# Optimization experiments

Measured on AMD Instinct MI355X. Metric: run time of the kernel, lower is better.

Reference implementation:

```python
import jax, jax.numpy as jnp
import numpy as np

N_NODES = 100000
N_EDGES = 1600000
F_IN = 128
F_OUT = 32


def setup_inputs() -> dict:
    key = jax.random.key(0)
    k1, k2, k3 = jax.random.split(key, 3)
    x = jax.random.normal(k1, (N_NODES, F_IN), dtype=jnp.float32)
    edge_index = jax.random.randint(k2, (2, N_EDGES), 0, N_NODES, dtype=jnp.int64)
    # Glorot-style init for the GCNConv linear weight [F_IN, F_OUT]
    W = jax.random.normal(k3, (F_IN, F_OUT), dtype=jnp.float32) * (1.0 / np.sqrt(F_IN))
    b = jnp.zeros((F_OUT,), dtype=jnp.float32)
    return {"x": x, "edge_index": edge_index, "W": W, "b": b}


def reference(x, edge_index, W, b):
    N = x.shape[0]
    # --- add self loops (PyG GCNConv default) ---
    loops = jnp.arange(N, dtype=edge_index.dtype)
    src = jnp.concatenate([edge_index[0], loops])  # message sources j
    dst = jnp.concatenate([edge_index[1], loops])  # aggregation targets i
    # --- symmetric normalization: deg^-1/2[src] * deg^-1/2[dst] ---
    ones = jnp.ones(src.shape[0], dtype=x.dtype)
    deg = jax.ops.segment_sum(ones, dst, num_segments=N)  # in-degree incl. self loop
    dinv = jnp.where(deg > 0, jax.lax.rsqrt(deg), jnp.zeros_like(deg))
    norm = dinv[src] * dinv[dst]  # [E+N]
    # --- linear transform then gather-scale-scatter aggregate ---
    h = x @ W  # [N, F_OUT]
    msgs = h[src] * norm[:, None]  # [E+N, F_OUT]
    out = jax.ops.segment_sum(msgs, dst, num_segments=N)  # [N, F_OUT]
    return out + b
```

## Files before the change

kernel.cpp:

```cpp
#include <hip/hip_runtime.h>
#include <hip/hip_fp16.h>

#define N_NODES 100000
#define N_EDGES 1600000
#define F_IN    128
#define F_OUT   32

#define BKT_SHIFT  7
#define BKT_SIZE   128
#define NBKT       782
#define BKT_STRIDE 2560

#define BIN_THREADS 512
#define BIN_TILE    8192
#define EPT         (BIN_TILE / BIN_THREADS)
#define NTILES      ((N_EDGES + BIN_TILE - 1) / BIN_TILE)

typedef _Float16 f16x8 __attribute__((ext_vector_type(8)));
typedef float    f32x4 __attribute__((ext_vector_type(4)));

__global__ __launch_bounds__(BIN_THREADS) void bin_kernel(const int* __restrict__ ei,
                                                          int* __restrict__ gcur,
                                                          unsigned int* __restrict__ binned) {
    __shared__ int cnt[NBKT], gbase[NBKT];
    int t = threadIdx.x;
    for (int b = t; b < NBKT; b += BIN_THREADS) cnt[b] = 0;
    __syncthreads();
    int ebase = blockIdx.x * BIN_TILE;
    unsigned int pk[EPT];
    int rk[EPT];
    short bkt[EPT];
#pragma unroll
    for (int k = 0; k < EPT; ++k) {
        int e = ebase + k * BIN_THREADS + t;
        if (e < N_EDGES) {
            int s = ei[e];
            int d = ei[N_EDGES + e];
            bkt[k] = (short)(d >> BKT_SHIFT);
            pk[k]  = (unsigned)s | ((unsigned)(d & (BKT_SIZE - 1)) << 25);
            rk[k]  = atomicAdd(&cnt[bkt[k]], 1);
        } else {
            bkt[k] = -1;
        }
    }
    __syncthreads();
    for (int b = t; b < NBKT; b += BIN_THREADS)
        if (cnt[b] > 0) gbase[b] = atomicAdd(&gcur[b], cnt[b]);
    __syncthreads();
#pragma unroll
    for (int k = 0; k < EPT; ++k) {
        if (bkt[k] >= 0) {
            int p = gbase[bkt[k]] + rk[k];
            if (p < BKT_STRIDE)
                binned[(size_t)bkt[k] * BKT_STRIDE + p] = pk[k];
        }
    }
}

#define WH_STRIDE 136
__global__ __launch_bounds__(512) void matmul_kernel(const float4* __restrict__ x4,
                                                     const float* __restrict__ W,
                                                     const unsigned int* __restrict__ binned,
                                                     const int* __restrict__ gcur,
                                                     __half* __restrict__ hs) {
    __shared__ _Float16 Wh[F_OUT * WH_STRIDE];
    __shared__ int cnt128[BKT_SIZE];
    __shared__ float dinvL[BKT_SIZE];
    int t = threadIdx.x;
    int b = blockIdx.x;

    if (t < BKT_SIZE) cnt128[t] = 0;
    {
        int col = t & 31, kb = (t >> 5) * 8;
        for (int u = 0; u < 8; ++u)
            Wh[col * WH_STRIDE + kb + u] = (_Float16)W[(kb + u) * F_OUT + col];
    }
    __syncthreads();

    int ne = gcur[b];
    if (ne > BKT_STRIDE) ne = BKT_STRIDE;
    const unsigned int* eb = binned + (size_t)b * BKT_STRIDE;
    for (int i = t; i < ne; i += 512)
        atomicAdd(&cnt128[eb[i] >> 25], 1);
    __syncthreads();
    if (t < BKT_SIZE) dinvL[t] = rsqrtf((float)(cnt128[t] + 1));
    __syncthreads();

    int w = t >> 6, l = t & 63;
    int lr = l & 15, kg = l >> 4;
    int row = b * 128 + w * 16 + lr;
    const float4* xr = x4 + (size_t)row * 32;
    bool rok = row < N_NODES;

    f16x8 a[4];
#pragma unroll
    for (int ks = 0; ks < 4; ++ks) {
        float4 v0, v1;
        if (rok) {
            v0 = xr[ks * 8 + kg * 2];
            v1 = xr[ks * 8 + kg * 2 + 1];
        } else {
            v0 = make_float4(0, 0, 0, 0);
            v1 = v0;
        }
        f16x8 av;
        av[0] = (_Float16)v0.x; av[1] = (_Float16)v0.y;
        av[2] = (_Float16)v0.z; av[3] = (_Float16)v0.w;
        av[4] = (_Float16)v1.x; av[5] = (_Float16)v1.y;
        av[6] = (_Float16)v1.z; av[7] = (_Float16)v1.w;
        a[ks] = av;
    }

    f32x4 c0 = {0.f, 0.f, 0.f, 0.f}, c1 = {0.f, 0.f, 0.f, 0.f};
#pragma unroll
    for (int ks = 0; ks < 4; ++ks) {
        f16x8 b0 = *(const f16x8*)&Wh[lr * WH_STRIDE + ks * 32 + kg * 8];
        f16x8 b1 = *(const f16x8*)&Wh[(16 + lr) * WH_STRIDE + ks * 32 + kg * 8];
        c0 = __builtin_amdgcn_mfma_f32_16x16x32_f16(a[ks], b0, c0, 0, 0, 0);
        c1 = __builtin_amdgcn_mfma_f32_16x16x32_f16(a[ks], b1, c1, 0, 0, 0);
    }

    int lrow0 = w * 16 + kg * 4;
#pragma unroll
    for (int i = 0; i < 4; ++i) {
        int orow = b * 128 + lrow0 + i;
        if (orow < N_NODES) {
            float dv = dinvL[lrow0 + i];
            hs[(size_t)orow * F_OUT + lr]      = (__half)(c0[i] * dv);
            hs[(size_t)orow * F_OUT + 16 + lr] = (__half)(c1[i] * dv);
        }
    }
}

__device__ inline void acc8(uint4 u, float* a) {
    float2 f0 = __half22float2(*(__half2*)&u.x);
    float2 f1 = __half22float2(*(__half2*)&u.y);
    float2 f2 = __half22float2(*(__half2*)&u.z);
    float2 f3 = __half22float2(*(__half2*)&u.w);
    a[0] += f0.x; a[1] += f0.y; a[2] += f1.x; a[3] += f1.y;
    a[4] += f2.x; a[5] += f2.y; a[6] += f3.x; a[7] += f3.y;
}

#define AEPT 5
__global__ __launch_bounds__(512) void aggregate_kernel(const unsigned int* __restrict__ binned,
                                                        const int* __restrict__ gcur,
                                                        const uint4* __restrict__ hs8,
                                                        const float* __restrict__ bias,
                                                        float* __restrict__ out) {
    __shared__ int cnt[BKT_SIZE];
    __shared__ int sc[BKT_SIZE];
    __shared__ int rp[BKT_SIZE + 1];
    __shared__ int se[BKT_STRIDE];
    int t = threadIdx.x;
    int b = blockIdx.x;
    int ne = gcur[b];
    if (ne > BKT_STRIDE) ne = BKT_STRIDE;
    const unsigned int* eb = binned + (size_t)b * BKT_STRIDE;

    if (t < BKT_SIZE) cnt[t] = 0;
    __syncthreads();

    unsigned pk[AEPT];
    int rk[AEPT];
#pragma unroll
    for (int k = 0; k < AEPT; ++k) {
        int i = t + k * 512;
        pk[k] = (i < ne) ? eb[i] : 0xFFFFFFFFu;
    }
#pragma unroll
    for (int k = 0; k < AEPT; ++k) {
        rk[k] = -1;
        if (pk[k] != 0xFFFFFFFFu)
            rk[k] = atomicAdd(&cnt[pk[k] >> 25], 1);
    }
    __syncthreads();
    int v = (t < BKT_SIZE) ? cnt[t] : 0;
    if (t < BKT_SIZE) sc[t] = v;
    __syncthreads();
    for (int off = 1; off < BKT_SIZE; off <<= 1) {
        int add = (t < BKT_SIZE && t >= off) ? sc[t - off] : 0;
        __syncthreads();
        if (t < BKT_SIZE) sc[t] += add;
        __syncthreads();
    }
    if (t < BKT_SIZE) rp[t] = sc[t] - v;
    if (t == 0) rp[BKT_SIZE] = ne;
    __syncthreads();
#pragma unroll
    for (int k = 0; k < AEPT; ++k) {
        if (rk[k] >= 0) {
            int pos = rp[pk[k] >> 25] + rk[k];
            se[pos] = (int)(pk[k] & 0x1FFFFFF);
        }
    }
    __syncthreads();

    int n = t >> 2, q = t & 3;
    int gnode = b * BKT_SIZE + n;
    if (gnode >= N_NODES) return;
    int beg = rp[n], end = rp[n + 1];
    int deg = end - beg;
    float acc[8] = {0.f, 0.f, 0.f, 0.f, 0.f, 0.f, 0.f, 0.f};
    int p = beg;
    for (; p + 7 < end; p += 8) {
        uint4 u0 = hs8[(size_t)se[p]     * 4 + q];
        uint4 u1 = hs8[(size_t)se[p + 1] * 4 + q];
        uint4 u2 = hs8[(size_t)se[p + 2] * 4 + q];
        uint4 u3 = hs8[(size_t)se[p + 3] * 4 + q];
        uint4 u4 = hs8[(size_t)se[p + 4] * 4 + q];
        uint4 u5 = hs8[(size_t)se[p + 5] * 4 + q];
        uint4 u6 = hs8[(size_t)se[p + 6] * 4 + q];
        uint4 u7 = hs8[(size_t)se[p + 7] * 4 + q];
        acc8(u0, acc); acc8(u1, acc); acc8(u2, acc); acc8(u3, acc);
        acc8(u4, acc); acc8(u5, acc); acc8(u6, acc); acc8(u7, acc);
    }
    for (; p + 3 < end; p += 4) {
        uint4 u0 = hs8[(size_t)se[p]     * 4 + q];
        uint4 u1 = hs8[(size_t)se[p + 1] * 4 + q];
        uint4 u2 = hs8[(size_t)se[p + 2] * 4 + q];
        uint4 u3 = hs8[(size_t)se[p + 3] * 4 + q];
        acc8(u0, acc); acc8(u1, acc); acc8(u2, acc); acc8(u3, acc);
    }
    for (; p < end; ++p)
        acc8(hs8[(size_t)se[p] * 4 + q], acc);

    float dv = rsqrtf((float)(deg + 1));
    uint4 us = hs8[(size_t)gnode * 4 + q];
    float selfv[8];
    {
        float2 f0 = __half22float2(*(__half2*)&us.x);
        float2 f1 = __half22float2(*(__half2*)&us.y);
        float2 f2 = __half22float2(*(__half2*)&us.z);
        float2 f3 = __half22float2(*(__half2*)&us.w);
        selfv[0] = f0.x; selfv[1] = f0.y; selfv[2] = f1.x; selfv[3] = f1.y;
        selfv[4] = f2.x; selfv[5] = f2.y; selfv[6] = f3.x; selfv[7] = f3.y;
    }
    float4 bv0 = *(const float4*)&bias[q * 8];
    float4 bv1 = *(const float4*)&bias[q * 8 + 4];
    float4 o0, o1;
    o0.x = bv0.x + dv * (acc[0] + selfv[0]);
    o0.y = bv0.y + dv * (acc[1] + selfv[1]);
    o0.z = bv0.z + dv * (acc[2] + selfv[2]);
    o0.w = bv0.w + dv * (acc[3] + selfv[3]);
    o1.x = bv1.x + dv * (acc[4] + selfv[4]);
    o1.y = bv1.y + dv * (acc[5] + selfv[5]);
    o1.z = bv1.z + dv * (acc[6] + selfv[6]);
    o1.w = bv1.w + dv * (acc[7] + selfv[7]);
    *(float4*)&out[(size_t)gnode * F_OUT + q * 8]     = o0;
    *(float4*)&out[(size_t)gnode * F_OUT + q * 8 + 4] = o1;
}

extern "C" void kernel_launch(void* const* d_in, const int* in_sizes, int n_in,
                              void* d_out, int out_size, void* d_ws, size_t ws_size,
                              hipStream_t stream) {
    const float* x  = (const float*)d_in[0];
    const int*   ei = (const int*)d_in[1];
    const float* W  = (const float*)d_in[2];
    const float* b  = (const float*)d_in[3];
    float* out = (float*)d_out;

    int*          gcur   = (int*)d_ws;
    unsigned int* binned = (unsigned int*)(gcur + 1024);
    __half*       hs     = (__half*)(binned + (size_t)NBKT * BKT_STRIDE);

    hipMemsetAsync(gcur, 0, NBKT * sizeof(int), stream);

    bin_kernel<<<NTILES, BIN_THREADS, 0, stream>>>(ei, gcur, binned);

    matmul_kernel<<<NBKT, 512, 0, stream>>>((const float4*)x, W, binned, gcur, hs);

    aggregate_kernel<<<NBKT, 512, 0, stream>>>(binned, gcur, (const uint4*)hs, b, out);
}
```

Measured before the change: 70.82 us.

## Co-schedule binning with matmul, split sort into own kernel, apply dinv per edge

```diff
diff --git a/kernel.cpp b/kernel.cpp
--- a/kernel.cpp
+++ b/kernel.cpp
@@ -10,147 +10,125 @@
 #define BKT_SIZE   128
 #define NBKT       782
 #define BKT_STRIDE 2560
+#define RP_STRIDE  132
 
 #define BIN_THREADS 512
 #define BIN_TILE    8192
-#define EPT         (BIN_TILE / BIN_THREADS)
+#define EPT         16
 #define NTILES      ((N_EDGES + BIN_TILE - 1) / BIN_TILE)
 
 typedef _Float16 f16x8 __attribute__((ext_vector_type(8)));
 typedef float    f32x4 __attribute__((ext_vector_type(4)));
 
-__global__ __launch_bounds__(BIN_THREADS) void bin_kernel(const int* __restrict__ ei,
-                                                          int* __restrict__ gcur,
-                                                          unsigned int* __restrict__ binned) {
-    __shared__ int cnt[NBKT], gbase[NBKT];
+#define WH_STRIDE 136
+
+__global__ __launch_bounds__(512) void fused_bin_matmul_kernel(const int* __restrict__ ei,
+                                                               int* __restrict__ gcur,
+                                                               unsigned int* __restrict__ binned,
+                                                               const float4* __restrict__ x4,
+                                                               const float* __restrict__ W,
+                                                               __half* __restrict__ hs) {
+    __shared__ char pool[9216];
     int t = threadIdx.x;
-    for (int b = t; b < NBKT; b += BIN_THREADS) cnt[b] = 0;
-    __syncthreads();
-    int ebase = blockIdx.x * BIN_TILE;
-    unsigned int pk[EPT];
-    int rk[EPT];
-    short bkt[EPT];
-#pragma unroll
-    for (int k = 0; k < EPT; ++k) {
-        int e = ebase + k * BIN_THREADS + t;
-        if (e < N_EDGES) {
-            int s = ei[e];
-            int d = ei[N_EDGES + e];
-            bkt[k] = (short)(d >> BKT_SHIFT);
-            pk[k]  = (unsigned)s | ((unsigned)(d & (BKT_SIZE - 1)) << 25);
-            rk[k]  = atomicAdd(&cnt[bkt[k]], 1);
-        } else {
-            bkt[k] = -1;
-        }
-    }
-    __syncthreads();
-    for (int b = t; b < NBKT; b += BIN_THREADS)
-        if (cnt[b] > 0) gbase[b] = atomicAdd(&gcur[b], cnt[b]);
-    __syncthreads();
-#pragma unroll
-    for (int k = 0; k < EPT; ++k) {
-        if (bkt[k] >= 0) {
-            int p = gbase[bkt[k]] + rk[k];
-            if (p < BKT_STRIDE)
-                binned[(size_t)bkt[k] * BKT_STRIDE + p] = pk[k];
-        }
-    }
-}
-
-#define WH_STRIDE 136
-__global__ __launch_bounds__(512) void matmul_kernel(const float4* __restrict__ x4,
-                                                     const float* __restrict__ W,
-                                                     const unsigned int* __restrict__ binned,
-                                                     const int* __restrict__ gcur,
-                                                     __half* __restrict__ hs) {
-    __shared__ _Float16 Wh[F_OUT * WH_STRIDE];
-    __shared__ int cnt128[BKT_SIZE];
-    __shared__ float dinvL[BKT_SIZE];
-    int t = threadIdx.x;
-    int b = blockIdx.x;
-
-    if (t < BKT_SIZE) cnt128[t] = 0;
-    {
-        int col = t & 31, kb = (t >> 5) * 8;
-        for (int u = 0; u < 8; ++u)
-            Wh[col * WH_STRIDE + kb + u] = (_Float16)W[(kb + u) * F_OUT + col];
-    }
-    __syncthreads();
-
-    int ne = gcur[b];
-    if (ne > BKT_STRIDE) ne = BKT_STRIDE;
-    const unsigned int* eb = binned + (size_t)b * BKT_STRIDE;
-    for (int i = t; i < ne; i += 512)
-        atomicAdd(&cnt128[eb[i] >> 25], 1);
-    __syncthreads();
-    if (t < BKT_SIZE) dinvL[t] = rsqrtf((float)(cnt128[t] + 1));
-    __syncthreads();
-
-    int w = t >> 6, l = t & 63;
-    int lr = l & 15, kg = l >> 4;
-    int row = b * 128 + w * 16 + lr;
-    const float4* xr = x4 + (size_t)row * 32;
-    bool rok = row < N_NODES;
-
-    f16x8 a[4];
-#pragma unroll
-    for (int ks = 0; ks < 4; ++ks) {
-        float4 v0, v1;
-        if (rok) {
-            v0 = xr[ks * 8 + kg * 2];
-            v1 = xr[ks * 8 + kg * 2 + 1];
-        } else {
-            v0 = make_float4(0, 0, 0, 0);
-            v1 = v0;
-        }
-        f16x8 av;
-        av[0] = (_Float16)v0.x; av[1] = (_Float16)v0.y;
-        av[2] = (_Float16)v0.z; av[3] = (_Float16)v0.w;
-        av[4] = (_Float16)v1.x; av[5] = (_Float16)v1.y;
-        av[6] = (_Float16)v1.z; av[7] = (_Float16)v1.w;
-        a[ks] = av;
-    }
-
-    f32x4 c0 = {0.f, 0.f, 0.f, 0.f}, c1 = {0.f, 0.f, 0.f, 0.f};
-#pragma unroll
-    for (int ks = 0; ks < 4; ++ks) {
-        f16x8 b0 = *(const f16x8*)&Wh[lr * WH_STRIDE + ks * 32 + kg * 8];
-        f16x8 b1 = *(const f16x8*)&Wh[(16 + lr) * WH_STRIDE + ks * 32 + kg * 8];
-        c0 = __builtin_amdgcn_mfma_f32_16x16x32_f16(a[ks], b0, c0, 0, 0, 0);
-        c1 = __builtin_amdgcn_mfma_f32_16x16x32_f16(a[ks], b1, c1, 0, 0, 0);
-    }
-
-    int lrow0 = w * 16 + kg * 4;
-#pragma unroll
-    for (int i = 0; i < 4; ++i) {
-        int orow = b * 128 + lrow0 + i;
-        if (orow < N_NODES) {
-            float dv = dinvL[lrow0 + i];
-            hs[(size_t)orow * F_OUT + lr]      = (__half)(c0[i] * dv);
-            hs[(size_t)orow * F_OUT + 16 + lr] = (__half)(c1[i] * dv);
-        }
-    }
-}
-
-__device__ inline void acc8(uint4 u, float* a) {
-    float2 f0 = __half22float2(*(__half2*)&u.x);
-    float2 f1 = __half22float2(*(__half2*)&u.y);
-    float2 f2 = __half22float2(*(__half2*)&u.z);
-    float2 f3 = __half22float2(*(__half2*)&u.w);
-    a[0] += f0.x; a[1] += f0.y; a[2] += f1.x; a[3] += f1.y;
-    a[4] += f2.x; a[5] += f2.y; a[6] += f3.x; a[7] += f3.y;
-}
-
-#define AEPT 5
-__global__ __launch_bounds__(512) void aggregate_kernel(const unsigned int* __restrict__ binned,
-                                                        const int* __restrict__ gcur,
-                                                        const uint4* __restrict__ hs8,
-                                                        const float* __restrict__ bias,
-                                                        float* __restrict__ out) {
+
+    if (blockIdx.x < NTILES) {
+        int* cnt   = (int*)pool;
+        int* gbase = cnt + NBKT;
+        for (int b = t; b < NBKT; b += BIN_THREADS) cnt[b] = 0;
+        __syncthreads();
+        int ebase = blockIdx.x * BIN_TILE;
+        unsigned int pk[EPT];
+        int rk[EPT];
+        short bkt[EPT];
+#pragma unroll
+        for (int k = 0; k < EPT; ++k) {
+            int e = ebase + k * BIN_THREADS + t;
+            if (e < N_EDGES) {
+                int s = ei[e];
+                int d = ei[N_EDGES + e];
+                bkt[k] = (short)(d >> BKT_SHIFT);
+                pk[k]  = (unsigned)s | ((unsigned)(d & (BKT_SIZE - 1)) << 25);
+                rk[k]  = atomicAdd(&cnt[bkt[k]], 1);
+            } else {
+                bkt[k] = -1;
+            }
+        }
+        __syncthreads();
+        for (int b = t; b < NBKT; b += BIN_THREADS)
+            if (cnt[b] > 0) gbase[b] = atomicAdd(&gcur[b], cnt[b]);
+        __syncthreads();
+#pragma unroll
+        for (int k = 0; k < EPT; ++k) {
+            if (bkt[k] >= 0) {
+                int p = gbase[bkt[k]] + rk[k];
+                if (p < BKT_STRIDE)
+                    binned[(size_t)bkt[k] * BKT_STRIDE + p] = pk[k];
+            }
+        }
+    } else {
+        _Float16* Wh = (_Float16*)pool;
+        int b = blockIdx.x - NTILES;
+        {
+            int col = t & 31, kb = (t >> 5) * 8;
+            for (int u = 0; u < 8; ++u)
+                Wh[col * WH_STRIDE + kb + u] = (_Float16)W[(kb + u) * F_OUT + col];
+        }
+        __syncthreads();
+
+        int w = t >> 6, l = t & 63;
+        int lr = l & 15, kg = l >> 4;
+        int row = b * 128 + w * 16 + lr;
+        const float4* xr = x4 + (size_t)row * 32;
+        bool rok = row < N_NODES;
+
+        f16x8 a[4];
+#pragma unroll
+        for (int ks = 0; ks < 4; ++ks) {
+            float4 v0, v1;
+            if (rok) {
+                v0 = xr[ks * 8 + kg * 2];
+                v1 = xr[ks * 8 + kg * 2 + 1];
+            } else {
+                v0 = make_float4(0, 0, 0, 0);
+                v1 = v0;
+            }
+            f16x8 av;
+            av[0] = (_Float16)v0.x; av[1] = (_Float16)v0.y;
+            av[2] = (_Float16)v0.z; av[3] = (_Float16)v0.w;
+            av[4] = (_Float16)v1.x; av[5] = (_Float16)v1.y;
+            av[6] = (_Float16)v1.z; av[7] = (_Float16)v1.w;
+            a[ks] = av;
+        }
+
+        f32x4 c0 = {0.f, 0.f, 0.f, 0.f}, c1 = {0.f, 0.f, 0.f, 0.f};
+#pragma unroll
+        for (int ks = 0; ks < 4; ++ks) {
+            f16x8 b0 = *(const f16x8*)&Wh[lr * WH_STRIDE + ks * 32 + kg * 8];
+            f16x8 b1 = *(const f16x8*)&Wh[(16 + lr) * WH_STRIDE + ks * 32 + kg * 8];
+            c0 = __builtin_amdgcn_mfma_f32_16x16x32_f16(a[ks], b0, c0, 0, 0, 0);
+            c1 = __builtin_amdgcn_mfma_f32_16x16x32_f16(a[ks], b1, c1, 0, 0, 0);
+        }
+
+        int lrow0 = w * 16 + kg * 4;
+#pragma unroll
+        for (int i = 0; i < 4; ++i) {
+            int orow = b * 128 + lrow0 + i;
+            if (orow < N_NODES) {
+                hs[(size_t)orow * F_OUT + lr]      = (__half)c0[i];
+                hs[(size_t)orow * F_OUT + 16 + lr] = (__half)c1[i];
+            }
+        }
+    }
+}
+
+__global__ __launch_bounds__(256) void sort_kernel(const unsigned int* __restrict__ binned,
+                                                   const int* __restrict__ gcur,
+                                                   int* __restrict__ se_g,
+                                                   int* __restrict__ rowptr,
+                                                   float* __restrict__ dinv) {
     __shared__ int cnt[BKT_SIZE];
     __shared__ int sc[BKT_SIZE];
     __shared__ int rp[BKT_SIZE + 1];
-    __shared__ int se[BKT_STRIDE];
     int t = threadIdx.x;
     int b = blockIdx.x;
     int ne = gcur[b];
@@ -160,15 +138,15 @@
     if (t < BKT_SIZE) cnt[t] = 0;
     __syncthreads();
 
-    unsigned pk[AEPT];
-    int rk[AEPT];
-#pragma unroll
-    for (int k = 0; k < AEPT; ++k) {
-        int i = t + k * 512;
+    unsigned pk[10];
+    int rk[10];
+#pragma unroll
+    for (int k = 0; k < 10; ++k) {
+        int i = t + k * 256;
         pk[k] = (i < ne) ? eb[i] : 0xFFFFFFFFu;
     }
 #pragma unroll
-    for (int k = 0; k < AEPT; ++k) {
+    for (int k = 0; k < 10; ++k) {
         rk[k] = -1;
         if (pk[k] != 0xFFFFFFFFu)
             rk[k] = atomicAdd(&cnt[pk[k] >> 25], 1);
@@ -186,68 +164,86 @@
     if (t < BKT_SIZE) rp[t] = sc[t] - v;
     if (t == 0) rp[BKT_SIZE] = ne;
     __syncthreads();
-#pragma unroll
-    for (int k = 0; k < AEPT; ++k) {
+
+    int gnode = b * BKT_SIZE + t;
+    if (t < BKT_SIZE && gnode < N_NODES)
+        dinv[gnode] = rsqrtf((float)(cnt[t] + 1));
+    if (t <= BKT_SIZE)
+        rowptr[b * RP_STRIDE + t] = rp[t];
+
+    int* se = se_g + (size_t)b * BKT_STRIDE;
+#pragma unroll
+    for (int k = 0; k < 10; ++k) {
         if (rk[k] >= 0) {
             int pos = rp[pk[k] >> 25] + rk[k];
             se[pos] = (int)(pk[k] & 0x1FFFFFF);
         }
     }
-    __syncthreads();
-
-    int n = t >> 2, q = t & 3;
+}
+
+__global__ __launch_bounds__(256) void aggregate_kernel(const int* __restrict__ se_g,
+                                                        const int* __restrict__ rowptr,
+                                                        const float* __restrict__ dinv,
+                                                        const uint2* __restrict__ hs4,
+                                                        const float* __restrict__ bias,
+                                                        float* __restrict__ out) {
+    int t = threadIdx.x;
+    int b   = blockIdx.x >> 2;
+    int sub = blockIdx.x & 3;
+    int n = sub * 32 + (t >> 3);
+    int j4 = t & 7;
     int gnode = b * BKT_SIZE + n;
     if (gnode >= N_NODES) return;
-    int beg = rp[n], end = rp[n + 1];
+    int beg = rowptr[b * RP_STRIDE + n];
+    int end = rowptr[b * RP_STRIDE + n + 1];
     int deg = end - beg;
-    float acc[8] = {0.f, 0.f, 0.f, 0.f, 0.f, 0.f, 0.f, 0.f};
+    const int* se = se_g + (size_t)b * BKT_STRIDE;
+
+    float a0 = 0.f, a1 = 0.f, a2 = 0.f, a3 = 0.f;
     int p = beg;
     for (; p + 7 < end; p += 8) {
-        uint4 u0 = hs8[(size_t)se[p]     * 4 + q];
-        uint4 u1 = hs8[(size_t)se[p + 1] * 4 + q];
-        uint4 u2 = hs8[(size_t)se[p + 2] * 4 + q];
-        uint4 u3 = hs8[(size_t)se[p + 3] * 4 + q];
-        uint4 u4 = hs8[(size_t)se[p + 4] * 4 + q];
-        uint4 u5 = hs8[(size_t)se[p + 5] * 4 + q];
-        uint4 u6 = hs8[(size_t)se[p + 6] * 4 + q];
-        uint4 u7 = hs8[(size_t)se[p + 7] * 4 + q];
-        acc8(u0, acc); acc8(u1, acc); acc8(u2, acc); acc8(u3, acc);
-        acc8(u4, acc); acc8(u5, acc); acc8(u6, acc); acc8(u7, acc);
-    }
-    for (; p + 3 < end; p += 4) {
-        uint4 u0 = hs8[(size_t)se[p]     * 4 + q];
-        uint4 u1 = hs8[(size_t)se[p + 1] * 4 + q];
-        uint4 u2 = hs8[(size_t)se[p + 2] * 4 + q];
-        uint4 u3 = hs8[(size_t)se[p + 3] * 4 + q];
-        acc8(u0, acc); acc8(u1, acc); acc8(u2, acc); acc8(u3, acc);
-    }
-    for (; p < end; ++p)
-        acc8(hs8[(size_t)se[p] * 4 + q], acc);
+        int s0 = se[p],     s1 = se[p + 1], s2 = se[p + 2], s3 = se[p + 3];
+        int s4 = se[p + 4], s5 = se[p + 5], s6 = se[p + 6], s7 = se[p + 7];
+        uint2 u0 = hs4[(size_t)s0 * 8 + j4]; float w0 = dinv[s0];
+        uint2 u1 = hs4[(size_t)s1 * 8 + j4]; float w1 = dinv[s1];
+        uint2 u2 = hs4[(size_t)s2 * 8 + j4]; float w2 = dinv[s2];
+        uint2 u3 = hs4[(size_t)s3 * 8 + j4]; float w3 = dinv[s3];
+        uint2 u4 = hs4[(size_t)s4 * 8 + j4]; float w4 = dinv[s4];
+        uint2 u5 = hs4[(size_t)s5 * 8 + j4]; float w5 = dinv[s5];
+        uint2 u6 = hs4[(size_t)s6 * 8 + j4]; float w6 = dinv[s6];
+        uint2 u7 = hs4[(size_t)s7 * 8 + j4]; float w7 = dinv[s7];
+#define FMA4(u, w) { \
+        float2 f0 = __half22float2(*(__half2*)&(u).x); \
+        float2 f1 = __half22float2(*(__half2*)&(u).y); \
+        a0 = fmaf(f0.x, (w), a0); a1 = fmaf(f0.y, (w), a1); \
+        a2 = fmaf(f1.x, (w), a2); a3 = fmaf(f1.y, (w), a3); }
+        FMA4(u0, w0) FMA4(u1, w1) FMA4(u2, w2) FMA4(u3, w3)
+        FMA4(u4, w4) FMA4(u5, w5) FMA4(u6, w6) FMA4(u7, w7)
+    }
+    for (; p + 1 < end; p += 2) {
+        int s0 = se[p], s1 = se[p + 1];
+        uint2 u0 = hs4[(size_t)s0 * 8 + j4]; float w0 = dinv[s0];
+        uint2 u1 = hs4[(size_t)s1 * 8 + j4]; float w1 = dinv[s1];
+        FMA4(u0, w0) FMA4(u1, w1)
+    }
+    if (p < end) {
+        int s0 = se[p];
+        uint2 u0 = hs4[(size_t)s0 * 8 + j4]; float w0 = dinv[s0];
+        FMA4(u0, w0)
+    }
+#undef FMA4
 
     float dv = rsqrtf((float)(deg + 1));
-    uint4 us = hs8[(size_t)gnode * 4 + q];
-    float selfv[8];
-    {
-        float2 f0 = __half22float2(*(__half2*)&us.x);
-        float2 f1 = __half22float2(*(__half2*)&us.y);
-        float2 f2 = __half22float2(*(__half2*)&us.z);
-        float2 f3 = __half22float2(*(__half2*)&us.w);
-        selfv[0] = f0.x; selfv[1] = f0.y; selfv[2] = f1.x; selfv[3] = f1.y;
-        selfv[4] = f2.x; selfv[5] = f2.y; selfv[6] = f3.x; selfv[7] = f3.y;
-    }
-    float4 bv0 = *(const float4*)&bias[q * 8];
-    float4 bv1 = *(const float4*)&bias[q * 8 + 4];
-    float4 o0, o1;
-    o0.x = bv0.x + dv * (acc[0] + selfv[0]);
-    o0.y = bv0.y + dv * (acc[1] + selfv[1]);
-    o0.z = bv0.z + dv * (acc[2] + selfv[2]);
-    o0.w = bv0.w + dv * (acc[3] + selfv[3]);
-    o1.x = bv1.x + dv * (acc[4] + selfv[4]);
-    o1.y = bv1.y + dv * (acc[5] + selfv[5]);
-    o1.z = bv1.z + dv * (acc[6] + selfv[6]);
-    o1.w = bv1.w + dv * (acc[7] + selfv[7]);
-    *(float4*)&out[(size_t)gnode * F_OUT + q * 8]     = o0;
-    *(float4*)&out[(size_t)gnode * F_OUT + q * 8 + 4] = o1;
+    uint2 us = hs4[(size_t)gnode * 8 + j4];
+    float2 s0 = __half22float2(*(__half2*)&us.x);
+    float2 s1 = __half22float2(*(__half2*)&us.y);
+    float4 bv = *(const float4*)&bias[j4 * 4];
+    float4 o;
+    o.x = bv.x + dv * (a0 + dv * s0.x);
+    o.y = bv.y + dv * (a1 + dv * s0.y);
+    o.z = bv.z + dv * (a2 + dv * s1.x);
+    o.w = bv.w + dv * (a3 + dv * s1.y);
+    *(float4*)&out[(size_t)gnode * F_OUT + j4 * 4] = o;
 }
 
 extern "C" void kernel_launch(void* const* d_in, const int* in_sizes, int n_in,
@@ -261,13 +257,17 @@
 
     int*          gcur   = (int*)d_ws;
     unsigned int* binned = (unsigned int*)(gcur + 1024);
-    __half*       hs     = (__half*)(binned + (size_t)NBKT * BKT_STRIDE);
+    int*          se_g   = (int*)(binned + (size_t)NBKT * BKT_STRIDE);
+    int*          rowptr = se_g + (size_t)NBKT * BKT_STRIDE;
+    float*        dinv   = (float*)(rowptr + NBKT * RP_STRIDE);
+    __half*       hs     = (__half*)(dinv + ((N_NODES + 3) & ~3));
 
     hipMemsetAsync(gcur, 0, NBKT * sizeof(int), stream);
 
-    bin_kernel<<<NTILES, BIN_THREADS, 0, stream>>>(ei, gcur, binned);
-
-    matmul_kernel<<<NBKT, 512, 0, stream>>>((const float4*)x, W, binned, gcur, hs);
-
-    aggregate_kernel<<<NBKT, 512, 0, stream>>>(binned, gcur, (const uint4*)hs, b, out);
-}
+    fused_bin_matmul_kernel<<<NTILES + NBKT, 512, 0, stream>>>(ei, gcur, binned,
+                                                               (const float4*)x, W, hs);
+
+    sort_kernel<<<NBKT, 256, 0, stream>>>(binned, gcur, se_g, rowptr, dinv);
+
+    aggregate_kernel<<<NBKT * 4, 256, 0, stream>>>(se_g, rowptr, dinv, (const uint2*)hs, b, out);
+}
```

New measurement: 80.31 us. 13.4% more time.

## Split aggregation of each bucket across two 256-thread blocks

Applied to the files above, without the earlier changes.

```diff
diff --git a/kernel.cpp b/kernel.cpp
--- a/kernel.cpp
+++ b/kernel.cpp
@@ -15,6 +15,10 @@
 #define BIN_TILE    8192
 #define EPT         (BIN_TILE / BIN_THREADS)
 #define NTILES      ((N_EDGES + BIN_TILE - 1) / BIN_TILE)
+
+#define AGG_SPLIT  2
+#define SUB        64
+#define SUB_STRIDE 1408
 
 typedef _Float16 f16x8 __attribute__((ext_vector_type(8)));
 typedef float    f32x4 __attribute__((ext_vector_type(4)));
@@ -141,65 +145,76 @@
     a[4] += f2.x; a[5] += f2.y; a[6] += f3.x; a[7] += f3.y;
 }
 
-#define AEPT 5
-__global__ __launch_bounds__(512) void aggregate_kernel(const unsigned int* __restrict__ binned,
+__global__ __launch_bounds__(256) void aggregate_kernel(const unsigned int* __restrict__ binned,
                                                         const int* __restrict__ gcur,
                                                         const uint4* __restrict__ hs8,
                                                         const float* __restrict__ bias,
                                                         float* __restrict__ out) {
-    __shared__ int cnt[BKT_SIZE];
-    __shared__ int sc[BKT_SIZE];
-    __shared__ int rp[BKT_SIZE + 1];
-    __shared__ int se[BKT_STRIDE];
+    __shared__ int cnt[SUB];
+    __shared__ int sc[SUB];
+    __shared__ int rp[SUB + 1];
+    __shared__ int se[SUB_STRIDE];
     int t = threadIdx.x;
-    int b = blockIdx.x;
+    int b   = blockIdx.x >> 1;
+    int sub = blockIdx.x & 1;
     int ne = gcur[b];
     if (ne > BKT_STRIDE) ne = BKT_STRIDE;
     const unsigned int* eb = binned + (size_t)b * BKT_STRIDE;
 
-    if (t < BKT_SIZE) cnt[t] = 0;
-    __syncthreads();
-
-    unsigned pk[AEPT];
-    int rk[AEPT];
-#pragma unroll
-    for (int k = 0; k < AEPT; ++k) {
-        int i = t + k * 512;
+    if (t < SUB) cnt[t] = 0;
+    __syncthreads();
+
+    unsigned pk[10];
+    int rk[10];
+#pragma unroll
+    for (int k = 0; k < 10; ++k) {
+        int i = t + k * 256;
         pk[k] = (i < ne) ? eb[i] : 0xFFFFFFFFu;
     }
 #pragma unroll
-    for (int k = 0; k < AEPT; ++k) {
+    for (int k = 0; k < 10; ++k) {
         rk[k] = -1;
-        if (pk[k] != 0xFFFFFFFFu)
-            rk[k] = atomicAdd(&cnt[pk[k] >> 25], 1);
-    }
-    __syncthreads();
-    int v = (t < BKT_SIZE) ? cnt[t] : 0;
-    if (t < BKT_SIZE) sc[t] = v;
-    __syncthreads();
-    for (int off = 1; off < BKT_SIZE; off <<= 1) {
-        int add = (t < BKT_SIZE && t >= off) ? sc[t - off] : 0;
+        if (pk[k] != 0xFFFFFFFFu) {
+            int dl = (int)(pk[k] >> 25);
+            if ((dl >> 6) == sub) rk[k] = atomicAdd(&cnt[dl & 63], 1);
+        }
+    }
+    __syncthreads();
+    int v = (t < SUB) ? cnt[t] : 0;
+    if (t < SUB) sc[t] = v;
+    __syncthreads();
+    for (int off = 1; off < SUB; off <<= 1) {
+        int add = (t < SUB && t >= off) ? sc[t - off] : 0;
         __syncthreads();
-        if (t < BKT_SIZE) sc[t] += add;
+        if (t < SUB) sc[t] += add;
         __syncthreads();
     }
-    if (t < BKT_SIZE) rp[t] = sc[t] - v;
-    if (t == 0) rp[BKT_SIZE] = ne;
-    __syncthreads();
-#pragma unroll
-    for (int k = 0; k < AEPT; ++k) {
+    if (t < SUB) {
+        int ex = sc[t] - v;
+        rp[t] = (ex < SUB_STRIDE) ? ex : SUB_STRIDE;
+    }
+    if (t == 0) {
+        int tot = sc[SUB - 1];
+        rp[SUB] = (tot > SUB_STRIDE) ? SUB_STRIDE : tot;
+    }
+    __syncthreads();
+#pragma unroll
+    for (int k = 0; k < 10; ++k) {
         if (rk[k] >= 0) {
-            int pos = rp[pk[k] >> 25] + rk[k];
-            se[pos] = (int)(pk[k] & 0x1FFFFFF);
+            int dl = (int)(pk[k] >> 25);
+            int pos = rp[dl & 63] + rk[k];
+            if (pos < SUB_STRIDE) se[pos] = (int)(pk[k] & 0x1FFFFFF);
         }
     }
     __syncthreads();
 
     int n = t >> 2, q = t & 3;
-    int gnode = b * BKT_SIZE + n;
+    int gnode = b * BKT_SIZE + sub * SUB + n;
     if (gnode >= N_NODES) return;
-    int beg = rp[n], end = rp[n + 1];
-    int deg = end - beg;
+    int deg = cnt[n];
+    int beg = rp[n];
+    int end = rp[n + 1];
+    if (beg + deg < end) end = beg + deg;
     float acc[8] = {0.f, 0.f, 0.f, 0.f, 0.f, 0.f, 0.f, 0.f};
     int p = beg;
     for (; p + 7 < end; p += 8) {
@@ -269,5 +284,5 @@
 
     matmul_kernel<<<NBKT, 512, 0, stream>>>((const float4*)x, W, binned, gcur, hs);
 
-    aggregate_kernel<<<NBKT, 512, 0, stream>>>(binned, gcur, (const uint4*)hs, b, out);
-}
+    aggregate_kernel<<<NBKT * AGG_SPLIT, 256, 0, stream>>>(binned, gcur, (const uint4*)hs, b, out);
+}
```

Measured after the change: 69.27 us. 2.2% less time.
